# Kernel tuning notes

Hardware: AMD Instinct MI355X
Metric: run time of the kernel (lower is better)

The kernel has to match this reference:

```python
import math
import jax, jax.numpy as jnp
import numpy as np

F0_BINS = 64; FRAME_HOP = 240; SR = 48000; LO_DIM = 16; N_HARM = 32
NOISE_FFT = 256; N_NOISE = NOISE_FFT // 2 + 1; VEL_DIM = 8
F0_MAX = 5000.0; F0_MIN = 20.0
B, T = 4, 500
NSAMP = T * FRAME_HOP
MLP, HID = 128, 64
FEAT = F0_BINS + LO_DIM + VEL_DIM  # 88


def _sincos_enc(norm, dim):
    # norm: (...,) in [0,1] -> (..., dim), even slots sin, odd slots cos
    i = jnp.arange(1, dim // 2 + 1, dtype=jnp.float32)
    ang = math.pi * i * norm[..., None]                    # (..., dim/2)
    return jnp.stack([jnp.sin(ang), jnp.cos(ang)], axis=-1).reshape(norm.shape + (dim,))


def lin_interp(x, out_len):
    # matches F.interpolate(mode='linear', align_corners=False); x: (..., Tin)
    Tin = x.shape[-1]
    pos = jnp.clip((jnp.arange(out_len, dtype=jnp.float32) + 0.5) * (Tin / out_len) - 0.5, 0.0, Tin - 1.0)
    i0 = jnp.floor(pos).astype(jnp.int32)
    i1 = jnp.minimum(i0 + 1, Tin - 1)
    w = pos - i0
    return x[..., i0] * (1.0 - w) + x[..., i1] * w


def _hann(n):
    return 0.5 - 0.5 * jnp.cos(2.0 * math.pi * jnp.arange(n, dtype=jnp.float32) / n)


def _stft(x, n_fft, hop, window):
    # torch.stft with center=True (reflect pad); returns (B, n_fft//2+1, n_frames)
    pad = n_fft // 2
    xp = jnp.pad(x, ((0, 0), (pad, pad)), mode='reflect')
    n_frames = 1 + (xp.shape[-1] - n_fft) // hop
    idx = jnp.arange(n_frames)[:, None] * hop + jnp.arange(n_fft)[None, :]
    frames = xp[:, idx] * window                           # (B, F, n_fft)
    return jnp.swapaxes(jnp.fft.rfft(frames, axis=-1), 1, 2)


def _istft(spec, n_fft, hop, window, length):
    frames = jnp.fft.irfft(jnp.swapaxes(spec, 1, 2), n=n_fft, axis=-1) * window  # (B, F, n_fft)
    nF = frames.shape[1]
    out_len = n_fft + hop * (nF - 1)
    idx = jnp.arange(nF)[:, None] * hop + jnp.arange(n_fft)[None, :]
    ola = jnp.zeros((frames.shape[0], out_len), frames.dtype).at[:, idx].add(frames)
    wsum = jnp.zeros((out_len,), frames.dtype).at[idx].add(jnp.broadcast_to(window ** 2, idx.shape))
    ola = ola / jnp.maximum(wsum, 1e-11)
    pad = n_fft // 2
    return ola[:, pad:pad + length]


def _gru(x, W_ih, W_hh, b_ih, b_hh):
    # torch nn.GRU, 1 layer, batch_first; gates ordered (r, z, n)
    H = W_hh.shape[1]
    def step(h, xt):
        gi = xt @ W_ih.T + b_ih
        gh = h @ W_hh.T + b_hh
        ir, iz, inn = jnp.split(gi, 3, axis=-1)
        hr, hz, hn = jnp.split(gh, 3, axis=-1)
        r = jax.nn.sigmoid(ir + hr)
        z = jax.nn.sigmoid(iz + hz)
        n = jnp.tanh(inn + r * hn)
        h_new = (1.0 - z) * n + z * h
        return h_new, h_new
    h0 = jnp.zeros((x.shape[0], H), x.dtype)
    _, ys = jax.lax.scan(step, h0, jnp.swapaxes(x, 0, 1))
    return jnp.swapaxes(ys, 0, 1)


def _harm_synth(harm_amps, overall_amp, f0_hz, n_samples):
    Bn, Tf, N = harm_amps.shape
    a = lin_interp(jnp.swapaxes(harm_amps, 1, 2), n_samples)      # (B, N, n)
    oa = lin_interp(jnp.swapaxes(overall_amp, 1, 2), n_samples)   # (B, 1, n)
    f0_up = lin_interp(f0_hz, n_samples)                          # (B, n)
    k = jnp.arange(1, N + 1, dtype=jnp.float32)
    inst_freq = f0_up[:, None, :] * k[None, :, None]              # (B, N, n)
    a = a * (inst_freq < SR * 0.45).astype(a.dtype)
    mean_freq = inst_freq.mean(axis=2, keepdims=True)             # (B, N, 1) -- faithful to source
    t = jnp.arange(n_samples, dtype=jnp.float32)
    phase = (2.0 * math.pi / SR) * mean_freq * t[None, None, :]
    return (a * jnp.sin(phase)).sum(axis=1, keepdims=True) * oa   # (B, 1, n)


def _noise_synth(noise_mags, noise, n_samples, n_fft=NOISE_FFT):
    hop = n_fft // 4
    window = _hann(n_fft)
    spec = _stft(noise, n_fft, hop, window)                       # (B, 129, T_stft)
    T_stft = spec.shape[-1]
    mag = lin_interp(jnp.swapaxes(noise_mags, 1, 2), T_stft)      # (B, 129, T_stft)
    return _istft(spec * mag, n_fft, hop, window, n_samples)[:, None, :]


def setup_inputs() -> dict:
    key = jax.random.key(0)
    ks = jax.random.split(key, 20)
    def lin(k, o, i, s=0.05):
        return jax.random.normal(k, (o, i), dtype=jnp.float32) * s
    inp = {
        'f0_hz': jax.random.uniform(ks[0], (B, T), jnp.float32) * 1980.0 + 20.0,
        'loudness_db': jax.random.uniform(ks[1], (B, T), jnp.float32) * -80.0,
        'velocity': jax.random.uniform(ks[2], (B,), jnp.float32) * 7.0,
        'noise_L': jax.random.normal(ks[3], (B, NSAMP), jnp.float32),
        'noise_R': jax.random.normal(ks[4], (B, NSAMP), jnp.float32),
        'W_pre1': lin(ks[5], MLP, FEAT), 'b_pre1': jnp.zeros((MLP,), jnp.float32),
        'W_pre2': lin(ks[6], MLP, MLP), 'b_pre2': jnp.zeros((MLP,), jnp.float32),
        'W_ih': lin(ks[7], 3 * HID, MLP), 'W_hh': lin(ks[8], 3 * HID, HID),
        'b_ih': jnp.zeros((3 * HID,), jnp.float32), 'b_hh': jnp.zeros((3 * HID,), jnp.float32),
        'W_post': lin(ks[9], MLP, HID), 'b_post': jnp.zeros((MLP,), jnp.float32),
        'W_hL': lin(ks[10], N_HARM, MLP), 'b_hL': jnp.zeros((N_HARM,), jnp.float32),
        'W_hR': lin(ks[11], N_HARM, MLP), 'b_hR': jnp.zeros((N_HARM,), jnp.float32),
        'W_amp': lin(ks[12], 1, MLP), 'b_amp': jnp.zeros((1,), jnp.float32),
        'W_nL': lin(ks[13], N_NOISE, MLP), 'b_nL': jnp.full((N_NOISE,), -3.0, jnp.float32),
        'W_nR': lin(ks[14], N_NOISE, MLP), 'b_nR': jnp.full((N_NOISE,), -3.0, jnp.float32),
    }
    return inp


def reference(f0_hz, loudness_db, velocity, noise_L, noise_R,
              W_pre1, b_pre1, W_pre2, b_pre2,
              W_ih, W_hh, b_ih, b_hh, W_post, b_post,
              W_hL, b_hL, W_hR, b_hR, W_amp, b_amp,
              W_nL, b_nL, W_nR, b_nR):
    Bn, Tn = f0_hz.shape
    # --- sinusoidal encodings ---
    f0_safe = jnp.clip(f0_hz, F0_MIN, None)
    f0_norm = jnp.clip((jnp.log(f0_safe) - math.log(F0_MIN)) / (math.log(F0_MAX) - math.log(F0_MIN)), 0.0, 1.0)
    f0_enc = _sincos_enc(f0_norm, F0_BINS) * (f0_hz > 0).astype(jnp.float32)[..., None]
    lo_enc = _sincos_enc(jnp.clip((loudness_db + 80.0) / 80.0, 0.0, 1.0), LO_DIM)
    vel_enc = _sincos_enc(jnp.clip(velocity / 7.0, 0.0, 1.0), VEL_DIM)  # (B, VEL_DIM)
    vel_enc = jnp.broadcast_to(vel_enc[:, None, :], (Bn, Tn, VEL_DIM))
    feat = jnp.concatenate([f0_enc, lo_enc, vel_enc], axis=-1)          # (B, T, 88)
    # --- trunk ---
    feat = jax.nn.relu(feat @ W_pre1.T + b_pre1)
    feat = jax.nn.relu(feat @ W_pre2.T + b_pre2)
    feat = _gru(feat, W_ih, W_hh, b_ih, b_hh)
    feat = jax.nn.relu(feat @ W_post.T + b_post)
    # --- heads ---
    harm_L = jax.nn.sigmoid(feat @ W_hL.T + b_hL)
    harm_R = jax.nn.sigmoid(feat @ W_hR.T + b_hR)
    overall_amp = jax.nn.softplus(feat @ W_amp.T + b_amp)               # (B, T, 1)
    nmag_L = jax.nn.sigmoid(feat @ W_nL.T + b_nL)
    nmag_R = jax.nn.sigmoid(feat @ W_nR.T + b_nR)
    n_samples = Tn * FRAME_HOP
    # --- synthesis ---
    L = _harm_synth(harm_L, overall_amp, f0_hz, n_samples) + _noise_synth(nmag_L, noise_L, n_samples)
    R = _harm_synth(harm_R, overall_amp, f0_hz, n_samples) + _noise_synth(nmag_R, noise_R, n_samples)
    return jnp.concatenate([L, R], axis=1)                              # (B, 2, n_samples)
```

## Files before the change

kernel.cpp:

```cpp
#include <hip/hip_runtime.h>
#include <math.h>

#ifndef M_PI
#define M_PI 3.14159265358979323846
#endif

#define BB 4
#define TT 500
#define NSAMP 120000
#define NHARM 32
#define NFFT 256
#define NBIN 129
#define NHOPF 64
#define NFRAMES 1876
#define HID 64
#define MLPD 128
#define FEATD 88

#define R_MAG ((float)(500.0/1876.0))
#define R_UP_F ((float)(500.0/120000.0))

typedef float v2f __attribute__((ext_vector_type(2)));

#define OFF_HARML 0
#define OFF_HARMR 64000
#define OFF_AMP   128000
#define OFF_NMAGL 130000
#define OFF_NMAGR 388000
#define OFF_C1    646000
#define OFF_H1    646128
#define OFF_GI    (OFF_H1+256000)
#define OFF_GOUT  (OFF_GI+384000)
#define OFF_SPECL (OFF_GOUT+128000)
#define OFF_SPECR (OFF_SPECL+4*NFRAMES*258)

__device__ __forceinline__ void up_coords(int m, int* i0, int* i1, float* w, float* w1){
  float pos = __fadd_rn(__fmul_rn(__fadd_rn((float)m, 0.5f), R_UP_F), -0.5f);
  pos = fminf(fmaxf(pos, 0.0f), 499.0f);
  int a = (int)pos;
  *i0 = a; *i1 = min(a+1, TT-1);
  float ww = __fsub_rn(pos, (float)a);
  *w = ww; *w1 = __fsub_rn(1.0f, ww);
}
__device__ __forceinline__ float f0_up_elem(const float* __restrict__ f0s, int m){
  int i0,i1; float w,w1;
  up_coords(m,&i0,&i1,&w,&w1);
  return __fadd_rn(__fmul_rn(f0s[i0], w1), __fmul_rn(f0s[i1], w));
}

__global__ __launch_bounds__(192) void k_front(const float* __restrict__ f0,
    const float* __restrict__ ldb, const float* __restrict__ vel,
    const float* __restrict__ Wp1, const float* __restrict__ bp1,
    const float* __restrict__ Wp2, const float* __restrict__ bp2,
    const float* __restrict__ Wih, const float* __restrict__ bih,
    float* __restrict__ gi){
  int row = blockIdx.x;
  int b = row / TT;
  int tid = threadIdx.x;
  __shared__ float feat[FEATD];
  __shared__ float h1s[MLPD];
  __shared__ float h2s[MLPD];
  if (tid < FEATD){
    float f = f0[row];
    float gate = (f > 0.0f) ? 1.0f : 0.0f;
    float fs = fmaxf(f, 20.0f);
    float fn = (logf(fs) - (float)2.995732273553991) / (float)5.5214609178622464;
    fn = fminf(fmaxf(fn, 0.0f), 1.0f);
    float ln = fminf(fmaxf((ldb[row] + 80.0f) / 80.0f, 0.0f), 1.0f);
    float vn = fminf(fmaxf(vel[b] / 7.0f, 0.0f), 1.0f);
    float norm; int i; float g2 = 1.0f;
    if (tid < 64){ i = (tid>>1) + 1; norm = fn; g2 = gate; }
    else if (tid < 80){ i = ((tid-64)>>1) + 1; norm = ln; }
    else { i = ((tid-80)>>1) + 1; norm = vn; }
    float ang = (float)M_PI * (float)i * norm;
    feat[tid] = ((tid & 1) ? cosf(ang) : sinf(ang)) * g2;
  }
  __syncthreads();
  if (tid < MLPD){
    const float* wp = Wp1 + tid*FEATD;
    float acc = bp1[tid];
    #pragma unroll 8
    for (int i=0;i<FEATD;i++) acc = fmaf(feat[i], wp[i], acc);
    h1s[tid] = fmaxf(acc, 0.0f);
  }
  __syncthreads();
  if (tid < MLPD){
    const float* wp = Wp2 + tid*MLPD;
    float acc = bp2[tid];
    #pragma unroll 8
    for (int i=0;i<MLPD;i++) acc = fmaf(h1s[i], wp[i], acc);
    h2s[tid] = fmaxf(acc, 0.0f);
  }
  __syncthreads();
  {
    const float* wp = Wih + tid*MLPD;
    float acc = bih[tid];
    #pragma unroll 8
    for (int i=0;i<MLPD;i++) acc = fmaf(h2s[i], wp[i], acc);
    gi[(size_t)row*192 + tid] = acc;
  }
}

__device__ float np_block_sum(const float* __restrict__ f0s, int off, int n, float kf){
  float r[8];
  #pragma unroll
  for (int j=0;j<8;j++) r[j] = __fmul_rn(f0_up_elem(f0s, off+j), kf);
  int lim = n - (n & 7);
  int i = 8;
  for (; i<lim; i+=8){
    #pragma unroll
    for (int j=0;j<8;j++)
      r[j] = __fadd_rn(r[j], __fmul_rn(f0_up_elem(f0s, off+i+j), kf));
  }
  float res = __fadd_rn(__fadd_rn(__fadd_rn(r[0],r[1]), __fadd_rn(r[2],r[3])),
                        __fadd_rn(__fadd_rn(r[4],r[5]), __fadd_rn(r[6],r[7])));
  for (; i<n; i++)
    res = __fadd_rn(res, __fmul_rn(f0_up_elem(f0s, off+i), kf));
  return res;
}

#define MID_GRU   BB
#define MID_MF    (MID_GRU + BB*32)
#define STFT_JOBS (2*BB*NFRAMES)
#define MID_STFT_BLOCKS ((STFT_JOBS+5)/6)
#define MID_BLOCKS (MID_MF + MID_STFT_BLOCKS)

#define RL(x,l) __uint_as_float(__builtin_amdgcn_readlane(__float_as_uint(x), (l)))

#define CH  25
#define NCH 20

__device__ __forceinline__ float fsig(float x){
  return __fdividef(1.0f, 1.0f + __expf(-x));
}
__device__ __forceinline__ float ftanh(float x){
  return fmaf(-2.0f, __fdividef(1.0f, 1.0f + __expf(2.0f*x)), 1.0f);
}

__global__
__attribute__((amdgpu_flat_work_group_size(384,384)))
__attribute__((amdgpu_waves_per_eu(2,2)))
void k_mid(
    const float* __restrict__ gi, const float* __restrict__ Whh,
    const float* __restrict__ bhh, float* __restrict__ gout,
    const float* __restrict__ f0, const float* __restrict__ nL,
    const float* __restrict__ nR, float* __restrict__ ws){
  __shared__ __align__(16) float sh[13696];
  int blk = blockIdx.x;
  int tid = threadIdx.x;

  if (blk < MID_GRU){
    float* gibuf = sh;
    float* hist  = sh + 9600;
    int b = blk;
    int j = tid & 63;
    v2f wr2[32], wz2[32], wn2[32];
    float br=0.f, bz=0.f, bn=0.f;
    if (tid < 64){
      #pragma unroll
      for (int i=0;i<16;i++){
        float4 a = *(const float4*)(Whh + (size_t)(j)*64     + i*4);
        float4 c = *(const float4*)(Whh + (size_t)(64+j)*64  + i*4);
        float4 d = *(const float4*)(Whh + (size_t)(128+j)*64 + i*4);
        wr2[2*i] = (v2f){a.x, a.y}; wr2[2*i+1] = (v2f){a.z, a.w};
        wz2[2*i] = (v2f){c.x, c.y}; wz2[2*i+1] = (v2f){c.z, c.w};
        wn2[2*i] = (v2f){d.x, d.y}; wn2[2*i+1] = (v2f){d.z, d.w};
      }
      br = bhh[j]; bz = bhh[64+j]; bn = bhh[128+j];
    }
    const float* gbase = gi + (size_t)b*TT*192;
    if (tid >= 64){
      int pt = tid - 64;
      for (int idx = pt; idx < CH*48; idx += 192){
        float4 v = *(const float4*)(gbase + idx*4);
        *(float4*)&gibuf[idx*4] = v;
      }
    }
    __syncthreads();
    float hreg = 0.0f;
    float* op = gout + (size_t)b*TT*64;
    for (int c=0; c<NCH; c++){
      if (tid >= 64){
        if (c+1 < NCH){
          int pt = tid - 64;
          const float* src = gbase + (size_t)(c+1)*CH*192;
          float* dst = &gibuf[((c+1)&1)*4800];
          for (int idx = pt; idx < CH*48; idx += 192){
            float4 v = *(const float4*)(src + idx*4);
            *(float4*)&dst[idx*4] = v;
          }
        }
      } else {
        const float* gch = &gibuf[(c&1)*4800];
        for (int tt=0; tt<CH; tt++){
          int t = c*CH + tt;
          float gr0 = gch[tt*192 + j];
          float gz0 = gch[tt*192 + 64 + j];
          float gn0 = gch[tt*192 + 128 + j];
          v2f AR0={0.f,0.f}, AR1={0.f,0.f};
          v2f AZ0={0.f,0.f}, AZ1={0.f,0.f};
          v2f AN0={0.f,0.f}, AN1={0.f,0.f};
          #pragma unroll
          for (int i=0;i<16;i++){
            v2f hA, hB;
            hA.x = RL(hreg, 2*i);    hA.y = RL(hreg, 2*i+1);
            hB.x = RL(hreg, 32+2*i); hB.y = RL(hreg, 33+2*i);
            AR0 = __builtin_elementwise_fma(wr2[i],    hA, AR0);
            AR1 = __builtin_elementwise_fma(wr2[16+i], hB, AR1);
            AZ0 = __builtin_elementwise_fma(wz2[i],    hA, AZ0);
            AZ1 = __builtin_elementwise_fma(wz2[16+i], hB, AZ1);
            AN0 = __builtin_elementwise_fma(wn2[i],    hA, AN0);
            AN1 = __builtin_elementwise_fma(wn2[16+i], hB, AN1);
          }
          float ar = __fadd_rn(__fadd_rn(AR0.x,AR0.y), __fadd_rn(AR1.x,AR1.y));
          float az = __fadd_rn(__fadd_rn(AZ0.x,AZ0.y), __fadd_rn(AZ1.x,AZ1.y));
          float an = __fadd_rn(__fadd_rn(AN0.x,AN0.y), __fadd_rn(AN1.x,AN1.y));
          float r = fsig(gr0 + ar + br);
          float z = fsig(gz0 + az + bz);
          float n = ftanh(gn0 + r*(an+bn));
          hreg = (1.0f - z)*n + z*hreg;
          int th = t & 63;
          hist[th*64 + j] = hreg;
          if (th == 63 || t == TT-1){
            int base_t = t - th;
            int per = th + 1;
            int nb = per >> 2;
            float* dst2 = op + base_t*64 + j*per;
            for (int q=0;q<nb;q++){
              float4 v = *(float4*)&hist[j*per + q*4];
              *(float4*)&dst2[q*4] = v;
            }
          }
        }
      }
      __syncthreads();
    }
  } else if (blk < MID_MF){
    int bk = blk - MID_GRU;
    int b = bk >> 5, k = bk & 31;
    float kf = (float)(k+1);
    float* f0s = sh;
    float* red = sh + 512;
    for (int i=tid;i<TT;i+=384) f0s[i] = f0[b*TT+i];
    __syncthreads();
    if (tid < 256){
      float lv[4];
      #pragma unroll
      for (int q=0;q<4;q++){
        int leafIdx = tid*4 + q;
        int off = 0, n = NSAMP;
        #pragma unroll
        for (int lvl=9; lvl>=0; --lvl){
          int n2 = (n>>1); n2 -= (n2 & 7);
          if ((leafIdx >> lvl) & 1){ off += n2; n -= n2; } else { n = n2; }
        }
        lv[q] = np_block_sum(f0s, off, n, kf);
      }
      red[tid] = __fadd_rn(__fadd_rn(lv[0],lv[1]), __fadd_rn(lv[2],lv[3]));
    }
    __syncthreads();
    for (int cnt=256; cnt>1; cnt>>=1){
      int half = cnt>>1;
      float v = 0.0f;
      if (tid < half) v = __fadd_rn(red[2*tid], red[2*tid+1]);
      __syncthreads();
      if (tid < half) red[tid] = v;
      __syncthreads();
    }
    if (tid==0){
      float mf = __fdiv_rn(red[0], 120000.0f);
      float c1 = __fmul_rn((float)(2.0*M_PI/48000.0), mf);
      ws[OFF_C1 + b*32 + k] = c1;
    }
  } else {
    int base = (blk - MID_MF)*6;
    int sub = tid >> 6;
    int j = tid & 63;
    float2* tw = (float2*)sh;
    float* frs = sh + 512 + sub*256;
    if (tid < 256){
      double a = (2.0*M_PI/256.0)*(double)tid;
      tw[tid] = make_float2((float)cos(a), (float)sin(a));
    }
    int jid = base + sub;
    bool act = jid < STFT_JOBS;
    int b=0, f=0; const float* x = nL;
    if (act){
      int ch = jid / (BB*NFRAMES);
      int rem = jid - ch*(BB*NFRAMES);
      b = rem / NFRAMES; f = rem - b*NFRAMES;
      x = (ch ? nR : nL) + (size_t)b*NSAMP;
      for (int n=j;n<256;n+=64){
        double a = (2.0*M_PI/256.0)*(double)n;
        int xi = f*NHOPF + n - 128;
        xi = xi < 0 ? -xi : xi;
        xi = xi >= NSAMP ? 2*(NSAMP-1)-xi : xi;
        float wnd = (float)(0.5 - 0.5*cos(a));
        frs[n] = x[xi]*wnd;
      }
    }
    __syncthreads();
    if (act){
      int ch = jid / (BB*NFRAMES);
      float* spec = ws + (ch ? OFF_SPECR : OFF_SPECL) + (size_t)(b*NFRAMES+f)*258;
      float re0=0.f, im0=0.f, re1=0.f, im1=0.f;
      int m0 = 0;
      #pragma unroll 4
      for (int n=0;n<256;n++){
        float fv = frs[n];
        int m1 = (m0 + ((n&3)<<6)) & 255;
        float2 t0 = tw[m0], t1 = tw[m1];
        re0 = fmaf(fv, t0.x, re0); im0 = fmaf(-fv, t0.y, im0);
        re1 = fmaf(fv, t1.x, re1); im1 = fmaf(-fv, t1.y, im1);
        m0 = (m0 + j) & 255;
      }
      float pq = frs[j] + frs[j+64] + frs[j+128] + frs[j+192];
      pq = (j & 1) ? -pq : pq;
      for (int o2=32;o2>0;o2>>=1) pq += __shfl_down(pq, o2, 64);
      spec[2*j]   = re0; spec[2*j+1]   = im0;
      spec[2*(j+64)] = re1; spec[2*(j+64)+1] = im1;
      if (j==0){ spec[256] = pq; spec[257] = 0.0f; }
    }
  }
}

__global__ __launch_bounds__(128) void k_posthead(const float* __restrict__ gout,
  const float* __restrict__ Wpo, const float* __restrict__ bpo,
  const float* __restrict__ WhL, const float* __restrict__ bhL,
  const float* __restrict__ WhR, const float* __restrict__ bhR,
  const float* __restrict__ Wam, const float* __restrict__ bam,
  const float* __restrict__ WnL, const float* __restrict__ bnL,
  const float* __restrict__ WnR, const float* __restrict__ bnR,
  float* __restrict__ harmL, float* __restrict__ harmR, float* __restrict__ amp,
  float* __restrict__ nmagL, float* __restrict__ nmagR){
  int row = blockIdx.x;
  int tid = threadIdx.x;
  __shared__ float gs[HID];
  __shared__ float post[MLPD];
  if (tid < HID) gs[tid] = gout[(size_t)row*HID + tid];
  __syncthreads();
  {
    const float* wp = Wpo + tid*HID;
    float acc = bpo[tid];
    #pragma unroll 8
    for (int i=0;i<HID;i++) acc = fmaf(gs[i], wp[i], acc);
    post[tid] = fmaxf(acc, 0.0f);
  }
  __syncthreads();
  #pragma unroll
  for (int rr=0;rr<3;rr++){
    int c = tid + rr*128;
    if (c >= 323) break;
    const float* W; const float* bb; float* o; int oc, ow; bool sp=false;
    if (c < 32)      { W=WhL; bb=bhL; o=harmL; oc=c;     ow=32; }
    else if (c < 64) { W=WhR; bb=bhR; o=harmR; oc=c-32;  ow=32; }
    else if (c == 64){ W=Wam; bb=bam; o=amp;   oc=0;     ow=1; sp=true; }
    else if (c < 194){ W=WnL; bb=bnL; o=nmagL; oc=c-65;  ow=129; }
    else             { W=WnR; bb=bnR; o=nmagR; oc=c-194; ow=129; }
    const float* wp = W + oc*MLPD;
    float acc = bb[oc];
    #pragma unroll 8
    for (int i=0;i<MLPD;i++) acc = fmaf(post[i], wp[i], acc);
    float v;
    if (sp) v = fmaxf(acc, 0.0f) + log1pf(expf(-fabsf(acc)));
    else    v = 1.0f/(1.0f+expf(-acc));
    o[(size_t)row*ow + oc] = v;
  }
}

__global__ __launch_bounds__(256) void k_istft(float* __restrict__ ws){
  int fr = blockIdx.x;
  int ch = blockIdx.y;
  int b = fr / NFRAMES, f = fr - b*NFRAMES;
  float* spec = ws + (ch ? OFF_SPECR : OFF_SPECL) + (size_t)fr*258;
  const float* nmag = ws + (ch ? OFF_NMAGR : OFF_NMAGL) + (size_t)b*TT*NBIN;
  int t = threadIdx.x;
  __shared__ float2 mx[NBIN];
  double a = (2.0*M_PI/256.0)*(double)t;
  float cz = (float)cos(a), sz = (float)sin(a);
  if (t < NBIN){
    float pos = ((float)f + 0.5f) * R_MAG - 0.5f;
    pos = fminf(fmaxf(pos, 0.0f), 499.0f);
    int i0 = (int)pos, i1 = min(i0+1, TT-1);
    float w = pos - (float)i0;
    float mg = nmag[i0*NBIN + t]*(1.0f-w) + nmag[i1*NBIN + t]*w;
    mx[t] = make_float2(spec[2*t]*mg, spec[2*t+1]*mg);
  }
  __syncthreads();
  float acc0 = mx[0].x + ((t&1) ? -mx[128].x : mx[128].x);
  float acc = 0.0f;
  float c = cz, s = sz;
  #pragma unroll 4
  for (int k=1;k<128;k++){
    float2 v = mx[k];
    acc = fmaf(v.x, c, acc);
    acc = fmaf(-v.y, s, acc);
    float ts_ = s*sz, tc_ = c*sz;
    float cn = fmaf(c, cz, -ts_);
    float sn = fmaf(s, cz,  tc_);
    c = cn; s = sn;
  }
  float y = (acc0 + 2.0f*acc) * (1.0f/256.0f);
  float win = 0.5f - 0.5f*cz;
  spec[t] = y*win;
}

__global__ __launch_bounds__(256) void k_out(const float* __restrict__ f0,
    const float* __restrict__ ws, float* __restrict__ out){
  __shared__ float win2[256];
  __shared__ float c1s[BB*32];
  {
    int t = threadIdx.x;
    double a = (2.0*M_PI/256.0)*(double)t;
    float w = (float)(0.5 - 0.5*cos(a));
    win2[t] = w*w;
    if (t < BB*32) c1s[t] = ws[OFF_C1 + t];
  }
  __syncthreads();
  int idx = blockIdx.x*256 + threadIdx.x;
  if (idx >= BB*2*NSAMP) return;
  int m = idx % NSAMP;
  int bc = idx / NSAMP;
  int ch = bc & 1, b = bc >> 1;
  int i0,i1; float w,w1;
  up_coords(m,&i0,&i1,&w,&w1);
  const float* f0b = f0 + b*TT;
  float f0u = __fadd_rn(__fmul_rn(f0b[i0], w1), __fmul_rn(f0b[i1], w));
  const float* am = ws + OFF_AMP + b*TT;
  float oa = __fadd_rn(__fmul_rn(am[i0], w1), __fmul_rn(am[i1], w));
  const float* ha = ws + (ch ? OFF_HARMR : OFF_HARML) + (size_t)b*TT*NHARM;
  float tm = (float)m;
  float hsum = 0.0f;
  for (int k=1;k<=NHARM;k++){
    float instf = __fmul_rn(f0u, (float)k);
    if (instf < 21600.0f){
      float a0 = ha[i0*NHARM + (k-1)], a1 = ha[i1*NHARM + (k-1)];
      float ak = __fadd_rn(__fmul_rn(a0, w1), __fmul_rn(a1, w));
      float ph = __fmul_rn(c1s[b*32 + (k-1)], tm);
      double rev = (double)ph * 0.15915494309189535;
      double fr2 = rev - floor(rev);
      float rad = (float)((fr2 - (fr2 >= 0.5 ? 1.0 : 0.0)) * 6.283185307179586);
      float s = sinf(rad);
      hsum = __fadd_rn(hsum, __fmul_rn(ak, s));
    }
  }
  float harm = __fmul_rn(hsum, oa);
  int p = m + 128;
  int fhi = min(p >> 6, NFRAMES-1);
  int flo = max((p - 192) >> 6, 0);
  const float* frb = ws + (ch ? OFF_SPECR : OFF_SPECL) + (size_t)b*NFRAMES*258;
  float nacc = 0.0f, wsum = 0.0f;
  for (int f=flo; f<=fhi; f++){
    int n = p - f*NHOPF;
    nacc += frb[f*258 + n];
    wsum += win2[n];
  }
  float noise = nacc / fmaxf(wsum, 1e-11f);
  out[idx] = __fadd_rn(harm, noise);
}

extern "C" void kernel_launch(void* const* d_in, const int* in_sizes, int n_in,
                              void* d_out, int out_size, void* d_ws, size_t ws_size,
                              hipStream_t stream){
  const float* f0  = (const float*)d_in[0];
  const float* ldb = (const float*)d_in[1];
  const float* vel = (const float*)d_in[2];
  const float* nL  = (const float*)d_in[3];
  const float* nR  = (const float*)d_in[4];
  const float* Wp1 = (const float*)d_in[5];
  const float* bp1 = (const float*)d_in[6];
  const float* Wp2 = (const float*)d_in[7];
  const float* bp2 = (const float*)d_in[8];
  const float* Wih = (const float*)d_in[9];
  const float* Whh = (const float*)d_in[10];
  const float* bih = (const float*)d_in[11];
  const float* bhh = (const float*)d_in[12];
  const float* Wpo = (const float*)d_in[13];
  const float* bpo = (const float*)d_in[14];
  const float* WhL = (const float*)d_in[15];
  const float* bhL = (const float*)d_in[16];
  const float* WhR = (const float*)d_in[17];
  const float* bhR = (const float*)d_in[18];
  const float* Wam = (const float*)d_in[19];
  const float* bam = (const float*)d_in[20];
  const float* WnL = (const float*)d_in[21];
  const float* bnL = (const float*)d_in[22];
  const float* WnR = (const float*)d_in[23];
  const float* bnR = (const float*)d_in[24];
  float* ws = (float*)d_ws;
  float* out = (float*)d_out;

  k_front<<<BB*TT, 192, 0, stream>>>(f0, ldb, vel, Wp1, bp1, Wp2, bp2, Wih, bih, ws+OFF_GI);
  k_mid<<<MID_BLOCKS, 384, 0, stream>>>(ws+OFF_GI, Whh, bhh, ws+OFF_GOUT, f0, nL, nR, ws);
  k_posthead<<<BB*TT, 128, 0, stream>>>(ws+OFF_GOUT, Wpo, bpo,
      WhL,bhL, WhR,bhR, Wam,bam, WnL,bnL, WnR,bnR,
      ws+OFF_HARML, ws+OFF_HARMR, ws+OFF_AMP, ws+OFF_NMAGL, ws+OFF_NMAGR);
  dim3 gs(BB*NFRAMES, 2);
  k_istft<<<gs, 256, 0, stream>>>(ws);
  k_out<<<(BB*2*NSAMP+255)/256, 256, 0, stream>>>(f0, ws, out);
}
```

Before: 433.1 us.

## Transpose weights once and batch multiple rows per block in MLP kernels

Adds a prep kernel that transposes the MLP and head weight matrices into the workspace so each thread reads them coalesced. The front and post-head kernels now process 10 and 8 rows per block respectively, reusing each loaded weight across several rows held in registers. The aim is to cut redundant uncoalesced weight traffic and the number of tiny blocks. It costs an extra launch and transpose on every call. The waves-per-EU hint on the GRU/STFT kernel is also loosened.

```diff
diff --git a/kernel.cpp b/kernel.cpp
--- a/kernel.cpp
+++ b/kernel.cpp
@@ -33,6 +33,13 @@
 #define OFF_GOUT  (OFF_GI+384000)
 #define OFF_SPECL (OFF_GOUT+128000)
 #define OFF_SPECR (OFF_SPECL+4*NFRAMES*258)
+#define WS_END0   (OFF_SPECR+4*NFRAMES*258)
+#define OFF_WT1   WS_END0
+#define OFF_WT2   (OFF_WT1+11264)
+#define OFF_WTIH  (OFF_WT2+16384)
+#define OFF_WTPO  (OFF_WTIH+24576)
+#define OFF_WTH   (OFF_WTPO+8192)
+#define PREP_TOT (11264+16384+24576+8192+41344)
 
 __device__ __forceinline__ void up_coords(int m, int* i0, int* i1, float* w, float* w1){
   float pos = __fadd_rn(__fmul_rn(__fadd_rn((float)m, 0.5f), R_UP_F), -0.5f);
@@ -48,56 +55,107 @@
   return __fadd_rn(__fmul_rn(f0s[i0], w1), __fmul_rn(f0s[i1], w));
 }
 
-__global__ __launch_bounds__(192) void k_front(const float* __restrict__ f0,
+__global__ __launch_bounds__(256) void k_prep(const float* __restrict__ Wp1,
+    const float* __restrict__ Wp2, const float* __restrict__ Wih,
+    const float* __restrict__ Wpo, const float* __restrict__ WhL,
+    const float* __restrict__ WhR, const float* __restrict__ Wam,
+    const float* __restrict__ WnL, const float* __restrict__ WnR,
+    float* __restrict__ ws){
+  int idx = blockIdx.x*256 + threadIdx.x;
+  if (idx >= PREP_TOT) return;
+  if (idx < 11264){ int i = idx >> 7, c = idx & 127; ws[OFF_WT1 + idx] = Wp1[c*FEATD + i]; return; }
+  idx -= 11264;
+  if (idx < 16384){ int i = idx >> 7, c = idx & 127; ws[OFF_WT2 + idx] = Wp2[c*MLPD + i]; return; }
+  idx -= 16384;
+  if (idx < 24576){ int i = idx / 192, c = idx - i*192; ws[OFF_WTIH + idx] = Wih[c*MLPD + i]; return; }
+  idx -= 24576;
+  if (idx < 8192){ int i = idx >> 7, c = idx & 127; ws[OFF_WTPO + idx] = Wpo[c*HID + i]; return; }
+  idx -= 8192;
+  { int i = idx / 323, c = idx - i*323;
+    float v;
+    if (c < 32)       v = WhL[c*MLPD + i];
+    else if (c < 64)  v = WhR[(c-32)*MLPD + i];
+    else if (c == 64) v = Wam[i];
+    else if (c < 194) v = WnL[(c-65)*MLPD + i];
+    else              v = WnR[(c-194)*MLPD + i];
+    ws[OFF_WTH + idx] = v; }
+}
+
+#define ROWS_F 10
+__global__ __launch_bounds__(256) void k_front(const float* __restrict__ f0,
     const float* __restrict__ ldb, const float* __restrict__ vel,
-    const float* __restrict__ Wp1, const float* __restrict__ bp1,
-    const float* __restrict__ Wp2, const float* __restrict__ bp2,
-    const float* __restrict__ Wih, const float* __restrict__ bih,
-    float* __restrict__ gi){
-  int row = blockIdx.x;
-  int b = row / TT;
+    const float* __restrict__ bp1, const float* __restrict__ bp2,
+    const float* __restrict__ bih, float* __restrict__ ws){
+  int r0 = blockIdx.x * ROWS_F;
   int tid = threadIdx.x;
-  __shared__ float feat[FEATD];
-  __shared__ float h1s[MLPD];
-  __shared__ float h2s[MLPD];
-  if (tid < FEATD){
+  __shared__ float norms[ROWS_F][4];
+  __shared__ float feat[ROWS_F][FEATD];
+  __shared__ float h1[ROWS_F][MLPD];
+  __shared__ float h2[ROWS_F][MLPD];
+  if (tid < ROWS_F){
+    int row = r0 + tid; int b = row / TT;
     float f = f0[row];
-    float gate = (f > 0.0f) ? 1.0f : 0.0f;
+    norms[tid][3] = (f > 0.0f) ? 1.0f : 0.0f;
     float fs = fmaxf(f, 20.0f);
     float fn = (logf(fs) - (float)2.995732273553991) / (float)5.5214609178622464;
-    fn = fminf(fmaxf(fn, 0.0f), 1.0f);
-    float ln = fminf(fmaxf((ldb[row] + 80.0f) / 80.0f, 0.0f), 1.0f);
-    float vn = fminf(fmaxf(vel[b] / 7.0f, 0.0f), 1.0f);
-    float norm; int i; float g2 = 1.0f;
-    if (tid < 64){ i = (tid>>1) + 1; norm = fn; g2 = gate; }
-    else if (tid < 80){ i = ((tid-64)>>1) + 1; norm = ln; }
-    else { i = ((tid-80)>>1) + 1; norm = vn; }
+    norms[tid][0] = fminf(fmaxf(fn, 0.0f), 1.0f);
+    norms[tid][1] = fminf(fmaxf((ldb[row] + 80.0f) / 80.0f, 0.0f), 1.0f);
+    norms[tid][2] = fminf(fmaxf(vel[b] / 7.0f, 0.0f), 1.0f);
+  }
+  __syncthreads();
+  for (int idx = tid; idx < ROWS_F*FEATD; idx += 256){
+    int r = idx / FEATD, e = idx - r*FEATD;
+    float norm, g2 = 1.0f; int i;
+    if (e < 64){ i = (e>>1)+1; norm = norms[r][0]; g2 = norms[r][3]; }
+    else if (e < 80){ i = ((e-64)>>1)+1; norm = norms[r][1]; }
+    else { i = ((e-80)>>1)+1; norm = norms[r][2]; }
     float ang = (float)M_PI * (float)i * norm;
-    feat[tid] = ((tid & 1) ? cosf(ang) : sinf(ang)) * g2;
-  }
-  __syncthreads();
-  if (tid < MLPD){
-    const float* wp = Wp1 + tid*FEATD;
-    float acc = bp1[tid];
-    #pragma unroll 8
-    for (int i=0;i<FEATD;i++) acc = fmaf(feat[i], wp[i], acc);
-    h1s[tid] = fmaxf(acc, 0.0f);
-  }
-  __syncthreads();
-  if (tid < MLPD){
-    const float* wp = Wp2 + tid*MLPD;
-    float acc = bp2[tid];
-    #pragma unroll 8
-    for (int i=0;i<MLPD;i++) acc = fmaf(h1s[i], wp[i], acc);
-    h2s[tid] = fmaxf(acc, 0.0f);
+    feat[r][e] = ((e & 1) ? cosf(ang) : sinf(ang)) * g2;
   }
   __syncthreads();
   {
-    const float* wp = Wih + tid*MLPD;
-    float acc = bih[tid];
-    #pragma unroll 8
-    for (int i=0;i<MLPD;i++) acc = fmaf(h2s[i], wp[i], acc);
-    gi[(size_t)row*192 + tid] = acc;
+    int c = tid & 127, rg = tid >> 7;
+    const float* wt = ws + OFF_WT1;
+    float acc[5];
+    #pragma unroll
+    for (int q=0;q<5;q++) acc[q] = bp1[c];
+    for (int i=0;i<FEATD;i++){
+      float w = wt[i*128 + c];
+      #pragma unroll
+      for (int q=0;q<5;q++) acc[q] = fmaf(feat[rg*5+q][i], w, acc[q]);
+    }
+    #pragma unroll
+    for (int q=0;q<5;q++) h1[rg*5+q][c] = fmaxf(acc[q], 0.0f);
+  }
+  __syncthreads();
+  {
+    int c = tid & 127, rg = tid >> 7;
+    const float* wt = ws + OFF_WT2;
+    float acc[5];
+    #pragma unroll
+    for (int q=0;q<5;q++) acc[q] = bp2[c];
+    for (int i=0;i<MLPD;i++){
+      float w = wt[i*128 + c];
+      #pragma unroll
+      for (int q=0;q<5;q++) acc[q] = fmaf(h1[rg*5+q][i], w, acc[q]);
+    }
+    #pragma unroll
+    for (int q=0;q<5;q++) h2[rg*5+q][c] = fmaxf(acc[q], 0.0f);
+  }
+  __syncthreads();
+  if (tid < 192){
+    const float* wt = ws + OFF_WTIH;
+    float* gi = ws + OFF_GI;
+    float acc[ROWS_F];
+    #pragma unroll
+    for (int r=0;r<ROWS_F;r++) acc[r] = bih[tid];
+    for (int i=0;i<MLPD;i++){
+      float w = wt[i*192 + tid];
+      #pragma unroll
+      for (int r=0;r<ROWS_F;r++) acc[r] = fmaf(h2[r][i], w, acc[r]);
+    }
+    #pragma unroll
+    for (int r=0;r<ROWS_F;r++) gi[(size_t)(r0+r)*192 + tid] = acc[r];
   }
 }
 
@@ -139,7 +197,7 @@
 
 __global__
 __attribute__((amdgpu_flat_work_group_size(384,384)))
-__attribute__((amdgpu_waves_per_eu(2,2)))
+__attribute__((amdgpu_waves_per_eu(1,4)))
 void k_mid(
     const float* __restrict__ gi, const float* __restrict__ Whh,
     const float* __restrict__ bhh, float* __restrict__ gout,
@@ -324,47 +382,57 @@
   }
 }
 
-__global__ __launch_bounds__(128) void k_posthead(const float* __restrict__ gout,
-  const float* __restrict__ Wpo, const float* __restrict__ bpo,
-  const float* __restrict__ WhL, const float* __restrict__ bhL,
-  const float* __restrict__ WhR, const float* __restrict__ bhR,
-  const float* __restrict__ Wam, const float* __restrict__ bam,
-  const float* __restrict__ WnL, const float* __restrict__ bnL,
-  const float* __restrict__ WnR, const float* __restrict__ bnR,
-  float* __restrict__ harmL, float* __restrict__ harmR, float* __restrict__ amp,
-  float* __restrict__ nmagL, float* __restrict__ nmagR){
-  int row = blockIdx.x;
+#define ROWS_P 8
+__global__ __launch_bounds__(384) void k_posthead(
+  const float* __restrict__ bpo,
+  const float* __restrict__ bhL, const float* __restrict__ bhR,
+  const float* __restrict__ bam, const float* __restrict__ bnL,
+  const float* __restrict__ bnR, float* __restrict__ ws){
+  int r0 = blockIdx.x * ROWS_P;
   int tid = threadIdx.x;
-  __shared__ float gs[HID];
-  __shared__ float post[MLPD];
-  if (tid < HID) gs[tid] = gout[(size_t)row*HID + tid];
+  __shared__ float gs[ROWS_P][HID];
+  __shared__ float post[ROWS_P][MLPD];
+  const float* gout = ws + OFF_GOUT;
+  for (int idx = tid; idx < ROWS_P*HID; idx += 384)
+    gs[idx>>6][idx&63] = gout[(size_t)(r0 + (idx>>6))*HID + (idx&63)];
   __syncthreads();
   {
-    const float* wp = Wpo + tid*HID;
-    float acc = bpo[tid];
-    #pragma unroll 8
-    for (int i=0;i<HID;i++) acc = fmaf(gs[i], wp[i], acc);
-    post[tid] = fmaxf(acc, 0.0f);
-  }
-  __syncthreads();
-  #pragma unroll
-  for (int rr=0;rr<3;rr++){
-    int c = tid + rr*128;
-    if (c >= 323) break;
-    const float* W; const float* bb; float* o; int oc, ow; bool sp=false;
-    if (c < 32)      { W=WhL; bb=bhL; o=harmL; oc=c;     ow=32; }
-    else if (c < 64) { W=WhR; bb=bhR; o=harmR; oc=c-32;  ow=32; }
-    else if (c == 64){ W=Wam; bb=bam; o=amp;   oc=0;     ow=1; sp=true; }
-    else if (c < 194){ W=WnL; bb=bnL; o=nmagL; oc=c-65;  ow=129; }
-    else             { W=WnR; bb=bnR; o=nmagR; oc=c-194; ow=129; }
-    const float* wp = W + oc*MLPD;
-    float acc = bb[oc];
-    #pragma unroll 8
-    for (int i=0;i<MLPD;i++) acc = fmaf(post[i], wp[i], acc);
-    float v;
-    if (sp) v = fmaxf(acc, 0.0f) + log1pf(expf(-fabsf(acc)));
-    else    v = 1.0f/(1.0f+expf(-acc));
-    o[(size_t)row*ow + oc] = v;
+    int c = tid & 127, rg = tid >> 7;
+    int rs = rg*3, nr = (rg==2)?2:3;
+    const float* wt = ws + OFF_WTPO;
+    float acc[3];
+    for (int q=0;q<nr;q++) acc[q] = bpo[c];
+    for (int i=0;i<HID;i++){
+      float w = wt[i*128 + c];
+      for (int q=0;q<nr;q++) acc[q] = fmaf(gs[rs+q][i], w, acc[q]);
+    }
+    for (int q=0;q<nr;q++) post[rs+q][c] = fmaxf(acc[q], 0.0f);
+  }
+  __syncthreads();
+  if (tid < 323){
+    int c = tid;
+    const float* wt = ws + OFF_WTH;
+    float bb; bool sp = false; float* o; int oc, ow;
+    if (c < 32)      { bb=bhL[c];      o=ws+OFF_HARML; oc=c;     ow=32; }
+    else if (c < 64) { bb=bhR[c-32];   o=ws+OFF_HARMR; oc=c-32;  ow=32; }
+    else if (c == 64){ bb=bam[0];      o=ws+OFF_AMP;   oc=0;     ow=1; sp=true; }
+    else if (c < 194){ bb=bnL[c-65];   o=ws+OFF_NMAGL; oc=c-65;  ow=129; }
+    else             { bb=bnR[c-194];  o=ws+OFF_NMAGR; oc=c-194; ow=129; }
+    float acc[ROWS_P];
+    #pragma unroll
+    for (int r=0;r<ROWS_P;r++) acc[r] = bb;
+    for (int i=0;i<MLPD;i++){
+      float w = wt[i*323 + c];
+      #pragma unroll
+      for (int r=0;r<ROWS_P;r++) acc[r] = fmaf(post[r][i], w, acc[r]);
+    }
+    #pragma unroll
+    for (int r=0;r<ROWS_P;r++){
+      float a = acc[r], v;
+      if (sp) v = fmaxf(a, 0.0f) + log1pf(expf(-fabsf(a)));
+      else    v = 1.0f/(1.0f+expf(-a));
+      o[(size_t)(r0+r)*ow + oc] = v;
+    }
   }
 }
 
@@ -490,11 +558,10 @@
   float* ws = (float*)d_ws;
   float* out = (float*)d_out;
 
-  k_front<<<BB*TT, 192, 0, stream>>>(f0, ldb, vel, Wp1, bp1, Wp2, bp2, Wih, bih, ws+OFF_GI);
+  k_prep<<<(PREP_TOT+255)/256, 256, 0, stream>>>(Wp1, Wp2, Wih, Wpo, WhL, WhR, Wam, WnL, WnR, ws);
+  k_front<<<BB*TT/ROWS_F, 256, 0, stream>>>(f0, ldb, vel, bp1, bp2, bih, ws);
   k_mid<<<MID_BLOCKS, 384, 0, stream>>>(ws+OFF_GI, Whh, bhh, ws+OFF_GOUT, f0, nL, nR, ws);
-  k_posthead<<<BB*TT, 128, 0, stream>>>(ws+OFF_GOUT, Wpo, bpo,
-      WhL,bhL, WhR,bhR, Wam,bam, WnL,bnL, WnR,bnR,
-      ws+OFF_HARML, ws+OFF_HARMR, ws+OFF_AMP, ws+OFF_NMAGL, ws+OFF_NMAGR);
+  k_posthead<<<BB*TT/ROWS_P, 384, 0, stream>>>(bpo, bhL, bhR, bam, bnL, bnR, ws);
   dim3 gs(BB*NFRAMES, 2);
   k_istft<<<gs, 256, 0, stream>>>(ws);
   k_out<<<(BB*2*NSAMP+255)/256, 256, 0, stream>>>(f0, ws, out);
```

Result: faster. 411.1 us (-5.1%).
